# Performance work log

Measured on AMD Instinct MI355X. Metric: run time of the kernel, lower is better.

## Reference

```python
import jax, jax.numpy as jnp
import numpy as np

N, E, D, H = 50000, 800000, 128, 8
HD = D // H  # 16
HID = 512
EPS = 1e-5
SLOPE = 0.2  # DGL GATConv default negative_slope


def setup_inputs() -> dict:
    key = jax.random.key(0)
    ks = jax.random.split(key, 10)
    s = 0.1
    return {
        "x": jax.random.normal(ks[0], (N, D), jnp.float32),
        "src": jax.random.randint(ks[1], (E,), 0, N),
        "dst": jax.random.randint(ks[2], (E,), 0, N),
        "W": jax.random.normal(ks[3], (D, D), jnp.float32) * s,
        "attn_l": jax.random.normal(ks[4], (H, HD), jnp.float32) * s,
        "attn_r": jax.random.normal(ks[5], (H, HD), jnp.float32) * s,
        "bias_gat": jnp.zeros((D,), jnp.float32),
        "bn1_gamma": jnp.ones((D,), jnp.float32),
        "bn1_beta": jnp.zeros((D,), jnp.float32),
        "W1": jax.random.normal(ks[6], (D, HID), jnp.float32) * s,
        "b1": jnp.zeros((HID,), jnp.float32),
        "W2": jax.random.normal(ks[7], (HID, D), jnp.float32) * s,
        "b2": jnp.zeros((D,), jnp.float32),
        "bn2_gamma": jnp.ones((D,), jnp.float32),
        "bn2_beta": jnp.zeros((D,), jnp.float32),
    }


def _batchnorm(v, gamma, beta):
    # BatchNorm1d, training-mode forward (batch statistics, biased var)
    mu = v.mean(0)
    var = v.var(0)
    return (v - mu) * jax.lax.rsqrt(var + EPS) * gamma + beta


def reference(x, src, dst, W, attn_l, attn_r, bias_gat,
              bn1_gamma, bn1_beta, W1, b1, W2, b2, bn2_gamma, bn2_beta):
    n = x.shape[0]
    # GATConv: project + per-head attention logits
    feat = (x @ W).reshape(n, H, HD)                     # [N, H, hd]
    el = jnp.einsum('nhd,hd->nh', feat, attn_l)          # [N, H]
    er = jnp.einsum('nhd,hd->nh', feat, attn_r)          # [N, H]
    e = el[src] + er[dst]                                # [E, H]
    e = jnp.where(e > 0, e, SLOPE * e)                   # LeakyReLU
    # segment (edge) softmax over incoming edges of each dst node
    m = jax.ops.segment_max(e, dst, num_segments=n)      # [N, H]
    ee = jnp.exp(e - m[dst])
    denom = jax.ops.segment_sum(ee, dst, num_segments=n)
    alpha = ee / denom[dst]                              # [E, H]
    # weighted scatter-aggregate of source features
    msg = feat[src] * alpha[:, :, None]                  # [E, H, hd]
    agg = jax.ops.segment_sum(msg, dst, num_segments=n)  # [N, H, hd]
    h = agg.reshape(n, D) + bias_gat
    # BN -> Linear -> ReLU -> Linear -> BN
    h = _batchnorm(h, bn1_gamma, bn1_beta)
    h = jax.nn.relu(h @ W1 + b1) @ W2 + b2
    h = _batchnorm(h, bn2_gamma, bn2_beta)
    return h
```

## Files before the change

### kernel.cpp

```cpp
#include <hip/hip_runtime.h>
#include <math.h>

#define NHEAD 8
#define DD 128
#define HIDD 512
#define NB 768

typedef _Float16 half8 __attribute__((ext_vector_type(8)));
typedef _Float16 half4 __attribute__((ext_vector_type(4)));
typedef float floatx4 __attribute__((ext_vector_type(4)));

__device__ __forceinline__ int swz256(int row, int bytecol) {
  return row * 256 + (bytecol ^ ((row & 15) << 4));
}
__device__ __forceinline__ int swz512(int row, int bytecol) {
  return row * 512 + (bytecol ^ ((row & 15) << 4));
}

__global__ __launch_bounds__(256) void pack_kernel(
    const float* __restrict__ W, const float* __restrict__ W1,
    const float* __restrict__ W2, _Float16* __restrict__ WP,
    _Float16* __restrict__ W1TP, _Float16* __restrict__ W2P)
{
  int i = blockIdx.x * 256 + threadIdx.x;
  if (i < 4 * 128 * 4 * 8) {
    int ii = i & 7, l4 = (i >> 3) & 3, col = (i >> 5) & 127, kc = i >> 12;
    WP[i] = (_Float16)W[(kc * 32 + l4 * 8 + ii) * DD + col];
  }
  if (i < 65536) {
    int ii = i & 7, e = (i >> 3) & 63, tile = i >> 9;
    int l4 = e >> 4, l15 = e & 15, hb = tile >> 2, kc = tile & 3;
    W1TP[i] = (_Float16)W1[(size_t)(kc * 32 + l4 * 8 + ii) * HIDD + hb * 16 + l15];
  }
  if (i < 65536) {
    int ii = i & 7, e = (i >> 3) & 63, tile = i >> 9;
    int l4 = e >> 4, l15 = e & 15, c = tile >> 3, cb = tile & 7;
    int hidden = (ii < 4) ? (2 * c) * 16 + 4 * l4 + ii
                          : (2 * c + 1) * 16 + 4 * l4 + (ii - 4);
    W2P[i] = (_Float16)W2[(size_t)hidden * DD + cb * 16 + l15];
  }
}

__global__ __launch_bounds__(256) void feat_mfma_kernel(
    const float* __restrict__ x, const _Float16* __restrict__ WP,
    _Float16* __restrict__ feat16, int N, int T)
{
  __shared__ char xs[32 * 512];
  const int tid = threadIdx.x;
  const int wv = tid >> 6, lane = tid & 63;
  const int l15 = lane & 15, l4 = lane >> 4;
  const int row = tid >> 3, seg = tid & 7;

  int t = blockIdx.x;
  float4 pre[4];
  {
    const int n = t * 32 + row;
    const bool ok = (t < T) && (n < N);
    const float4* sp = (const float4*)(x + (size_t)n * DD + seg * 16);
    const float4 z = make_float4(0.f, 0.f, 0.f, 0.f);
    #pragma unroll
    for (int c = 0; c < 4; ++c) pre[c] = ok ? sp[c] : z;
  }

  for (; t < T; t += NB) {
    const int n0 = t * 32;
    #pragma unroll
    for (int c = 0; c < 4; ++c)
      *(float4*)(xs + swz512(row, seg * 64 + c * 16)) = pre[c];
    __syncthreads();

    floatx4 acc[2][2];
    #pragma unroll
    for (int mf = 0; mf < 2; ++mf) { acc[mf][0] = (floatx4)0.f; acc[mf][1] = (floatx4)0.f; }

    #pragma unroll
    for (int kc = 0; kc < 4; ++kc) {
      half8 b0 = *(const half8*)(WP + ((kc * 128 + wv * 32 + l15) * 4 + l4) * 8);
      half8 b1 = *(const half8*)(WP + ((kc * 128 + wv * 32 + 16 + l15) * 4 + l4) * 8);
      #pragma unroll
      for (int mf = 0; mf < 2; ++mf) {
        const int rr = mf * 16 + l15;
        float4 a0 = *(const float4*)(xs + swz512(rr, kc * 128 + l4 * 32));
        float4 a1 = *(const float4*)(xs + swz512(rr, kc * 128 + l4 * 32 + 16));
        half8 af;
        af[0] = (_Float16)a0.x; af[1] = (_Float16)a0.y; af[2] = (_Float16)a0.z; af[3] = (_Float16)a0.w;
        af[4] = (_Float16)a1.x; af[5] = (_Float16)a1.y; af[6] = (_Float16)a1.z; af[7] = (_Float16)a1.w;
        acc[mf][0] = __builtin_amdgcn_mfma_f32_16x16x32_f16(af, b0, acc[mf][0], 0, 0, 0);
        acc[mf][1] = __builtin_amdgcn_mfma_f32_16x16x32_f16(af, b1, acc[mf][1], 0, 0, 0);
      }
    }

    {
      const int tn = t + NB;
      const int n = tn * 32 + row;
      const bool ok = (tn < T) && (n < N);
      const float4* sp = (const float4*)(x + (size_t)n * DD + seg * 16);
      const float4 z = make_float4(0.f, 0.f, 0.f, 0.f);
      #pragma unroll
      for (int c = 0; c < 4; ++c) pre[c] = ok ? sp[c] : z;
    }

    #pragma unroll
    for (int mf = 0; mf < 2; ++mf) {
      #pragma unroll
      for (int r = 0; r < 4; ++r) {
        const int rown = n0 + mf * 16 + l4 * 4 + r;
        if (rown < N) {
          feat16[(size_t)rown * DD + wv * 32 + l15] = (_Float16)acc[mf][0][r];
          feat16[(size_t)rown * DD + wv * 32 + 16 + l15] = (_Float16)acc[mf][1][r];
        }
      }
    }
    __syncthreads();
  }
}

__global__ __launch_bounds__(256) void elr_kernel(
    const _Float16* __restrict__ feat16, const float* __restrict__ attn_l,
    const float* __restrict__ attn_r, float* __restrict__ el,
    float* __restrict__ er, int N)
{
  int gid = blockIdx.x * 256 + threadIdx.x;
  if (gid >= N * NHEAD) return;
  const int n = gid >> 3, h = gid & 7;
  const half8* fp = (const half8*)(feat16 + (size_t)n * DD + h * 16);
  half8 f0 = fp[0], f1 = fp[1];
  float sl = 0.f, sr = 0.f;
  #pragma unroll
  for (int d = 0; d < 8; ++d) {
    float v0 = (float)f0[d], v1 = (float)f1[d];
    sl = fmaf(v0, attn_l[h * 16 + d], sl);
    sl = fmaf(v1, attn_l[h * 16 + 8 + d], sl);
    sr = fmaf(v0, attn_r[h * 16 + d], sr);
    sr = fmaf(v1, attn_r[h * 16 + 8 + d], sr);
  }
  el[gid] = sl;
  er[gid] = sr;
}

__global__ __launch_bounds__(256) void count_kernel(const int* __restrict__ dst,
                                                    int* __restrict__ counts,
                                                    int* __restrict__ rank, int E)
{
  int e = blockIdx.x * 256 + threadIdx.x;
  if (e < E) rank[e] = atomicAdd(&counts[dst[e]], 1);
}

__global__ __launch_bounds__(256) void scan1_kernel(const int* __restrict__ counts,
                                                    int* __restrict__ offsets,
                                                    int* __restrict__ btot)
{
  __shared__ int wsum[4];
  const int lane = threadIdx.x & 63;
  const int wid = threadIdx.x >> 6;
  int4 c = *(const int4*)(counts + blockIdx.x * 1024 + threadIdx.x * 4);
  int q = c.x + c.y + c.z + c.w;
  int incl = q;
  #pragma unroll
  for (int d = 1; d < 64; d <<= 1) {
    int t = __shfl_up(incl, d, 64);
    if (lane >= d) incl += t;
  }
  if (lane == 63) wsum[wid] = incl;
  __syncthreads();
  int wprefix = 0;
  for (int w = 0; w < wid; ++w) wprefix += wsum[w];
  int excl = wprefix + incl - q;
  int4 o;
  o.x = excl; o.y = excl + c.x; o.z = o.y + c.y; o.w = o.z + c.z;
  *(int4*)(offsets + blockIdx.x * 1024 + threadIdx.x * 4) = o;
  if (threadIdx.x == 0) btot[blockIdx.x] = wsum[0] + wsum[1] + wsum[2] + wsum[3];
}

__global__ __launch_bounds__(64) void scan2_kernel(const int* __restrict__ btot,
                                                   int* __restrict__ bof, int nchunk)
{
  const int t = threadIdx.x;
  const int K = (nchunk + 63) >> 6;
  const int base = t * K;
  int s = 0;
  for (int i = 0; i < K; ++i) if (base + i < nchunk) s += btot[base + i];
  int incl = s;
  #pragma unroll
  for (int d = 1; d < 64; d <<= 1) {
    int tt = __shfl_up(incl, d, 64);
    if (t >= d) incl += tt;
  }
  int run = incl - s;
  for (int i = 0; i < K; ++i) if (base + i < nchunk) { bof[base + i] = run; run += btot[base + i]; }
}

__global__ __launch_bounds__(256) void fill_kernel(const int* __restrict__ src,
                                                   const int* __restrict__ dst,
                                                   const int* __restrict__ offsets,
                                                   const int* __restrict__ bof,
                                                   const int* __restrict__ rank,
                                                   int* __restrict__ srcl, int E)
{
  int e = blockIdx.x * 256 + threadIdx.x;
  if (e < E) {
    int d = dst[e];
    srcl[offsets[d] + bof[d >> 10] + rank[e]] = src[e];
  }
}

__global__ __launch_bounds__(256) void agg_kernel(
    const _Float16* __restrict__ feat16, const float* __restrict__ el,
    const float* __restrict__ er, const int* __restrict__ offsets,
    const int* __restrict__ bof, const int* __restrict__ srcl,
    const float* __restrict__ bias, float* __restrict__ hout, int N)
{
  int gid = blockIdx.x * 256 + threadIdx.x;
  if (gid >= N * 16) return;
  const int n = gid >> 4;
  const int sub = gid & 15;
  const int hh = sub >> 1;
  const int half = sub & 1;
  const int o0 = offsets[n] + bof[n >> 10];
  const int o1 = offsets[n + 1] + bof[(n + 1) >> 10];
  const int cnt = o1 - o0;
  const int mid = o0 + ((cnt + 1) >> 1);
  int j = half ? mid : o0;
  const int je = half ? o1 : mid;
  const float er_nh = er[n * NHEAD + hh];

  float s = 0.f;
  float a[16];
  #pragma unroll
  for (int d = 0; d < 16; ++d) a[d] = 0.f;

  for (; j + 1 < je; j += 2) {
    const int s0 = srcl[j], s1 = srcl[j + 1];
    float e0 = el[s0 * NHEAD + hh] + er_nh;
    float e1 = el[s1 * NHEAD + hh] + er_nh;
    const half8* f0p = (const half8*)(feat16 + (size_t)s0 * DD + hh * 16);
    const half8* f1p = (const half8*)(feat16 + (size_t)s1 * DD + hh * 16);
    e0 = e0 > 0.f ? e0 : 0.2f * e0;
    e1 = e1 > 0.f ? e1 : 0.2f * e1;
    const float pp0 = __expf(e0);
    const float pp1 = __expf(e1);
    half8 f00 = f0p[0], f01 = f0p[1];
    half8 f10 = f1p[0], f11 = f1p[1];
    s += pp0 + pp1;
    #pragma unroll
    for (int d = 0; d < 8; ++d) {
      a[d]     = fmaf(pp0, (float)f00[d], fmaf(pp1, (float)f10[d], a[d]));
      a[d + 8] = fmaf(pp0, (float)f01[d], fmaf(pp1, (float)f11[d], a[d + 8]));
    }
  }
  if (j < je) {
    const int s0 = srcl[j];
    float e0 = el[s0 * NHEAD + hh] + er_nh;
    e0 = e0 > 0.f ? e0 : 0.2f * e0;
    const float pp0 = __expf(e0);
    const half8* f0p = (const half8*)(feat16 + (size_t)s0 * DD + hh * 16);
    half8 f00 = f0p[0], f01 = f0p[1];
    s += pp0;
    #pragma unroll
    for (int d = 0; d < 8; ++d) {
      a[d]     = fmaf(pp0, (float)f00[d], a[d]);
      a[d + 8] = fmaf(pp0, (float)f01[d], a[d + 8]);
    }
  }

  s += __shfl_xor(s, 1, 64);
  #pragma unroll
  for (int d = 0; d < 16; ++d) a[d] += __shfl_xor(a[d], 1, 64);

  const float inv = (cnt > 0) ? 1.f / s : 0.f;
  const int cbase = hh * 16 + half * 8;
  float* op = hout + (size_t)n * DD + cbase;
  const float* bp = bias + cbase;
  const int abase = half * 8;
  float4 o0v, o1v;
  o0v.x = fmaf(a[abase + 0], inv, bp[0]);
  o0v.y = fmaf(a[abase + 1], inv, bp[1]);
  o0v.z = fmaf(a[abase + 2], inv, bp[2]);
  o0v.w = fmaf(a[abase + 3], inv, bp[3]);
  o1v.x = fmaf(a[abase + 4], inv, bp[4]);
  o1v.y = fmaf(a[abase + 5], inv, bp[5]);
  o1v.z = fmaf(a[abase + 6], inv, bp[6]);
  o1v.w = fmaf(a[abase + 7], inv, bp[7]);
  *(float4*)(op) = o0v;
  *(float4*)(op + 4) = o1v;
}

__global__ __launch_bounds__(256) void bnstats_kernel(
    const float* __restrict__ h, float* __restrict__ sums,
    float* __restrict__ sumsq, int N)
{
  __shared__ float rs[256], rss[256];
  const int c = threadIdx.x & 127;
  const int half = threadIdx.x >> 7;
  const int rowsPer = (N + gridDim.x - 1) / gridDim.x;
  const int r0 = blockIdx.x * rowsPer;
  const int r1 = min(N, r0 + rowsPer);
  float s = 0.f, ss = 0.f;
  for (int r = r0 + half; r < r1; r += 2) {
    float v = h[(size_t)r * DD + c];
    s += v; ss += v * v;
  }
  rs[threadIdx.x] = s; rss[threadIdx.x] = ss;
  __syncthreads();
  if (threadIdx.x < 128) {
    s = rs[threadIdx.x] + rs[threadIdx.x + 128];
    ss = rss[threadIdx.x] + rss[threadIdx.x + 128];
    atomicAdd(&sums[c], s);
    atomicAdd(&sumsq[c], ss);
  }
}

__global__ __launch_bounds__(128, 2) void mlp_mfma_kernel(
    const float* __restrict__ hbuf, const float* __restrict__ sum1,
    const float* __restrict__ ss1, const float* __restrict__ bn1_g,
    const float* __restrict__ bn1_b, const _Float16* __restrict__ W1TP,
    const _Float16* __restrict__ W2P, const float* __restrict__ b1,
    const float* __restrict__ b2, float* __restrict__ out, int N)
{
  __shared__ char myA[8192];
  __shared__ char xch[8192];
  const int tid = threadIdx.x;
  const int wv = tid >> 6;
  const int lane = tid & 63;
  const int l15 = lane & 15, l4 = lane >> 4;
  const int n0 = blockIdx.x * 32;
  if (n0 >= N) return;

  {
    const int c0 = (tid & 31) * 4;
    const int rq = tid >> 5;
    float sc[4], sh[4];
    #pragma unroll
    for (int jj = 0; jj < 4; ++jj) {
      float mean = sum1[c0 + jj] / (float)N;
      float var = ss1[c0 + jj] / (float)N - mean * mean;
      float s = bn1_g[c0 + jj] * rsqrtf(var + 1e-5f);
      sc[jj] = s; sh[jj] = bn1_b[c0 + jj] - mean * s;
    }
    #pragma unroll
    for (int it = 0; it < 8; ++it) {
      const int row = it * 4 + rq;
      const int n = n0 + row;
      float4 v = make_float4(0.f, 0.f, 0.f, 0.f);
      if (n < N) v = *(const float4*)(hbuf + (size_t)n * DD + c0);
      half4 hv;
      hv[0] = (_Float16)fmaf(v.x, sc[0], sh[0]);
      hv[1] = (_Float16)fmaf(v.y, sc[1], sh[1]);
      hv[2] = (_Float16)fmaf(v.z, sc[2], sh[2]);
      hv[3] = (_Float16)fmaf(v.w, sc[3], sh[3]);
      *(half4*)(myA + swz256(row, c0 * 2)) = hv;
    }
  }
  __syncthreads();

  half8 xf[2][4];
  #pragma unroll
  for (int nb = 0; nb < 2; ++nb)
    #pragma unroll
    for (int kc = 0; kc < 4; ++kc)
      xf[nb][kc] = *(const half8*)(myA + swz256(nb * 16 + l15, kc * 64 + l4 * 16));

  floatx4 acc2[2][8];
  #pragma unroll
  for (int nb = 0; nb < 2; ++nb)
    #pragma unroll
    for (int cb = 0; cb < 8; ++cb) acc2[nb][cb] = (floatx4)0.f;

  half8 a2s[8][2];
  #pragma unroll
  for (int c8 = 0; c8 < 8; ++c8) {
    const int c = wv * 8 + c8;
    floatx4 dA[2], dB[2];
    dA[0] = (floatx4)0.f; dA[1] = (floatx4)0.f;
    dB[0] = (floatx4)0.f; dB[1] = (floatx4)0.f;
    half8 wA[4], wB[4];
    #pragma unroll
    for (int kc = 0; kc < 4; ++kc) {
      wA[kc] = *(const half8*)(W1TP + (size_t)((2 * c) * 4 + kc) * 512 + (l4 * 16 + l15) * 8);
      wB[kc] = *(const half8*)(W1TP + (size_t)((2 * c + 1) * 4 + kc) * 512 + (l4 * 16 + l15) * 8);
    }
    __builtin_amdgcn_s_setprio(1);
    #pragma unroll
    for (int kc = 0; kc < 4; ++kc) {
      dA[0] = __builtin_amdgcn_mfma_f32_16x16x32_f16(wA[kc], xf[0][kc], dA[0], 0, 0, 0);
      dA[1] = __builtin_amdgcn_mfma_f32_16x16x32_f16(wA[kc], xf[1][kc], dA[1], 0, 0, 0);
      dB[0] = __builtin_amdgcn_mfma_f32_16x16x32_f16(wB[kc], xf[0][kc], dB[0], 0, 0, 0);
      dB[1] = __builtin_amdgcn_mfma_f32_16x16x32_f16(wB[kc], xf[1][kc], dB[1], 0, 0, 0);
    }
    __builtin_amdgcn_s_setprio(0);
    floatx4 bA = *(const floatx4*)&b1[(2 * c) * 16 + l4 * 4];
    floatx4 bB = *(const floatx4*)&b1[(2 * c + 1) * 16 + l4 * 4];
    #pragma unroll
    for (int nb = 0; nb < 2; ++nb) {
      #pragma unroll
      for (int r = 0; r < 4; ++r) {
        float vA = dA[nb][r] + bA[r];
        float vB = dB[nb][r] + bB[r];
        a2s[c8][nb][r]     = (_Float16)(vA > 0.f ? vA : 0.f);
        a2s[c8][nb][r + 4] = (_Float16)(vB > 0.f ? vB : 0.f);
      }
    }
  }
  #pragma unroll
  for (int c8 = 0; c8 < 8; ++c8) {
    const int c = wv * 8 + c8;
    half8 w2[8];
    #pragma unroll
    for (int cb = 0; cb < 8; ++cb)
      w2[cb] = *(const half8*)(W2P + (size_t)(c * 8 + cb) * 512 + (l4 * 16 + l15) * 8);
    __builtin_amdgcn_s_setprio(1);
    #pragma unroll
    for (int cb = 0; cb < 8; ++cb) {
      acc2[0][cb] = __builtin_amdgcn_mfma_f32_16x16x32_f16(a2s[c8][0], w2[cb], acc2[0][cb], 0, 0, 0);
      acc2[1][cb] = __builtin_amdgcn_mfma_f32_16x16x32_f16(a2s[c8][1], w2[cb], acc2[1][cb], 0, 0, 0);
    }
    __builtin_amdgcn_s_setprio(0);
  }

  if (wv == 1) {
    #pragma unroll
    for (int nb = 0; nb < 2; ++nb) {
      #pragma unroll
      for (int cb = 0; cb < 8; ++cb) {
        half4 hv;
        #pragma unroll
        for (int r = 0; r < 4; ++r) hv[r] = (_Float16)acc2[nb][cb][r];
        *(half4*)(xch + ((nb * 8 + cb) * 64 + lane) * 8) = hv;
      }
    }
  }
  __syncthreads();
  if (wv == 0) {
    float b2v[8];
    #pragma unroll
    for (int cb = 0; cb < 8; ++cb) b2v[cb] = b2[cb * 16 + l15];
    #pragma unroll
    for (int nb = 0; nb < 2; ++nb) {
      #pragma unroll
      for (int cb = 0; cb < 8; ++cb) {
        half4 hv = *(const half4*)(xch + ((nb * 8 + cb) * 64 + lane) * 8);
        #pragma unroll
        for (int r = 0; r < 4; ++r) acc2[nb][cb][r] += (float)hv[r];
      }
    }
    #pragma unroll
    for (int nb = 0; nb < 2; ++nb) {
      #pragma unroll
      for (int r = 0; r < 4; ++r) {
        const int rown = n0 + nb * 16 + l4 * 4 + r;
        if (rown < N) {
          #pragma unroll
          for (int cb = 0; cb < 8; ++cb)
            out[(size_t)rown * DD + cb * 16 + l15] = acc2[nb][cb][r] + b2v[cb];
        }
      }
    }
  }
}

__global__ __launch_bounds__(256) void applybn_kernel(
    float* __restrict__ out, const float* __restrict__ sum2,
    const float* __restrict__ ss2, const float* __restrict__ gamma,
    const float* __restrict__ beta, int N, int total4)
{
  __shared__ float sc[128], sh[128];
  if (threadIdx.x < 128) {
    int c = threadIdx.x;
    float mean = sum2[c] / (float)N;
    float var = ss2[c] / (float)N - mean * mean;
    float s = gamma[c] * rsqrtf(var + 1e-5f);
    sc[c] = s;
    sh[c] = beta[c] - mean * s;
  }
  __syncthreads();
  int i = blockIdx.x * 256 + threadIdx.x;
  const int stride = gridDim.x * 256;
  for (; i < total4; i += stride) {
    float4 v = ((float4*)out)[i];
    int c = (i & 31) * 4;
    float4 scv = *(const float4*)&sc[c];
    float4 shv = *(const float4*)&sh[c];
    v.x = fmaf(v.x, scv.x, shv.x); v.y = fmaf(v.y, scv.y, shv.y);
    v.z = fmaf(v.z, scv.z, shv.z); v.w = fmaf(v.w, scv.w, shv.w);
    ((float4*)out)[i] = v;
  }
}

extern "C" void kernel_launch(void* const* d_in, const int* in_sizes, int n_in,
                              void* d_out, int out_size, void* d_ws, size_t ws_size,
                              hipStream_t stream) {
  const float* x        = (const float*)d_in[0];
  const int*   src      = (const int*)d_in[1];
  const int*   dst      = (const int*)d_in[2];
  const float* W        = (const float*)d_in[3];
  const float* attn_l   = (const float*)d_in[4];
  const float* attn_r   = (const float*)d_in[5];
  const float* bias_gat = (const float*)d_in[6];
  const float* bn1_g    = (const float*)d_in[7];
  const float* bn1_b    = (const float*)d_in[8];
  const float* W1       = (const float*)d_in[9];
  const float* b1       = (const float*)d_in[10];
  const float* W2       = (const float*)d_in[11];
  const float* b2       = (const float*)d_in[12];
  const float* bn2_g    = (const float*)d_in[13];
  const float* bn2_b    = (const float*)d_in[14];
  float* out = (float*)d_out;

  const int N = in_sizes[0] / DD;
  const int E = in_sizes[1];
  const int NPAD = ((N + 1023) / 1024) * 1024;
  const int NCHUNK = NPAD / 1024;
  const int T = (N + 31) / 32;

  _Float16* feat16 = (_Float16*)d_ws;
  float* hbuf = (float*)(feat16 + (size_t)((N + 1) & ~1) * DD);
  float* el   = hbuf + (size_t)N * DD;
  float* er   = el + (size_t)N * NHEAD;
  int* counts = (int*)(er + (size_t)N * NHEAD);
  int* offsets = counts + NPAD;
  int* srcl   = offsets + NPAD;
  int* btot   = srcl + E;
  int* bof    = btot + 64;
  float* stats = (float*)(bof + 64);
  float* sum1 = stats, *ss1 = stats + 128;
  float* sum2 = stats + 256, *ss2 = stats + 384;
  _Float16* WP   = (_Float16*)(stats + 1024);
  _Float16* W1TP = WP + 4 * 128 * 32;
  _Float16* W2P  = W1TP + 65536;
  int* rank = (int*)hbuf;

  hipMemsetAsync(counts, 0, (size_t)NPAD * sizeof(int), stream);
  hipMemsetAsync(stats, 0, 512 * sizeof(float), stream);

  pack_kernel<<<256, 256, 0, stream>>>(W, W1, W2, WP, W1TP, W2P);
  feat_mfma_kernel<<<NB, 256, 0, stream>>>(x, WP, feat16, N, T);
  elr_kernel<<<(N * NHEAD + 255) / 256, 256, 0, stream>>>(feat16, attn_l, attn_r, el, er, N);
  count_kernel<<<(E + 255) / 256, 256, 0, stream>>>(dst, counts, rank, E);
  scan1_kernel<<<NCHUNK, 256, 0, stream>>>(counts, offsets, btot);
  scan2_kernel<<<1, 64, 0, stream>>>(btot, bof, NCHUNK);
  fill_kernel<<<(E + 255) / 256, 256, 0, stream>>>(src, dst, offsets, bof, rank, srcl, E);
  agg_kernel<<<(N * 16 + 255) / 256, 256, 0, stream>>>(feat16, el, er, offsets, bof,
                                                       srcl, bias_gat, hbuf, N);
  bnstats_kernel<<<256, 256, 0, stream>>>(hbuf, sum1, ss1, N);
  mlp_mfma_kernel<<<T, 128, 0, stream>>>(hbuf, sum1, ss1, bn1_g, bn1_b, W1TP, W2P,
                                         b1, b2, out, N);
  bnstats_kernel<<<256, 256, 0, stream>>>(out, sum2, ss2, N);
  applybn_kernel<<<2048, 256, 0, stream>>>(out, sum2, ss2, bn2_g, bn2_b, N, N * DD / 4);
}
```

Before: 230.1 us.

## Unroll GAT aggregation by four edges and split MLP hidden dim across four waves

The edge aggregation loop now handles four source edges per iteration instead of two, putting more independent gathers in flight per thread. The MLP kernel goes from two to four waves per block, each owning a quarter of the 512 hidden units. This halves per-wave MFMA and register work, and the three non-leader waves reduce their partial outputs through a larger shared-memory exchange buffer. The cost is three times the LDS for the exchange, a longer serial reduction in wave 0, and extra fp16 rounding of partials.

```diff
diff --git a/kernel.cpp b/kernel.cpp
--- a/kernel.cpp
+++ b/kernel.cpp
@@ -229,37 +229,46 @@
   #pragma unroll
   for (int d = 0; d < 16; ++d) a[d] = 0.f;
 
-  for (; j + 1 < je; j += 2) {
-    const int s0 = srcl[j], s1 = srcl[j + 1];
+  for (; j + 3 < je; j += 4) {
+    const int s0 = srcl[j], s1 = srcl[j + 1], s2 = srcl[j + 2], s3 = srcl[j + 3];
     float e0 = el[s0 * NHEAD + hh] + er_nh;
     float e1 = el[s1 * NHEAD + hh] + er_nh;
+    float e2 = el[s2 * NHEAD + hh] + er_nh;
+    float e3 = el[s3 * NHEAD + hh] + er_nh;
     const half8* f0p = (const half8*)(feat16 + (size_t)s0 * DD + hh * 16);
     const half8* f1p = (const half8*)(feat16 + (size_t)s1 * DD + hh * 16);
+    const half8* f2p = (const half8*)(feat16 + (size_t)s2 * DD + hh * 16);
+    const half8* f3p = (const half8*)(feat16 + (size_t)s3 * DD + hh * 16);
     e0 = e0 > 0.f ? e0 : 0.2f * e0;
     e1 = e1 > 0.f ? e1 : 0.2f * e1;
-    const float pp0 = __expf(e0);
-    const float pp1 = __expf(e1);
+    e2 = e2 > 0.f ? e2 : 0.2f * e2;
+    e3 = e3 > 0.f ? e3 : 0.2f * e3;
+    const float p0 = __expf(e0), p1 = __expf(e1), p2 = __expf(e2), p3 = __expf(e3);
     half8 f00 = f0p[0], f01 = f0p[1];
     half8 f10 = f1p[0], f11 = f1p[1];
-    s += pp0 + pp1;
+    half8 f20 = f2p[0], f21 = f2p[1];
+    half8 f30 = f3p[0], f31 = f3p[1];
+    s += (p0 + p1) + (p2 + p3);
     #pragma unroll
     for (int d = 0; d < 8; ++d) {
-      a[d]     = fmaf(pp0, (float)f00[d], fmaf(pp1, (float)f10[d], a[d]));
-      a[d + 8] = fmaf(pp0, (float)f01[d], fmaf(pp1, (float)f11[d], a[d + 8]));
-    }
-  }
-  if (j < je) {
+      float t0 = fmaf(p0, (float)f00[d], fmaf(p1, (float)f10[d], a[d]));
+      a[d] = fmaf(p2, (float)f20[d], fmaf(p3, (float)f30[d], t0));
+      float t1 = fmaf(p0, (float)f01[d], fmaf(p1, (float)f11[d], a[d + 8]));
+      a[d + 8] = fmaf(p2, (float)f21[d], fmaf(p3, (float)f31[d], t1));
+    }
+  }
+  for (; j < je; ++j) {
     const int s0 = srcl[j];
     float e0 = el[s0 * NHEAD + hh] + er_nh;
     e0 = e0 > 0.f ? e0 : 0.2f * e0;
-    const float pp0 = __expf(e0);
+    const float p0 = __expf(e0);
     const half8* f0p = (const half8*)(feat16 + (size_t)s0 * DD + hh * 16);
     half8 f00 = f0p[0], f01 = f0p[1];
-    s += pp0;
+    s += p0;
     #pragma unroll
     for (int d = 0; d < 8; ++d) {
-      a[d]     = fmaf(pp0, (float)f00[d], a[d]);
-      a[d + 8] = fmaf(pp0, (float)f01[d], a[d + 8]);
+      a[d]     = fmaf(p0, (float)f00[d], a[d]);
+      a[d + 8] = fmaf(p0, (float)f01[d], a[d + 8]);
     }
   }
 
@@ -310,7 +319,7 @@
   }
 }
 
-__global__ __launch_bounds__(128, 2) void mlp_mfma_kernel(
+__global__ __launch_bounds__(256, 2) void mlp_mfma_kernel(
     const float* __restrict__ hbuf, const float* __restrict__ sum1,
     const float* __restrict__ ss1, const float* __restrict__ bn1_g,
     const float* __restrict__ bn1_b, const _Float16* __restrict__ W1TP,
@@ -318,7 +327,7 @@
     const float* __restrict__ b2, float* __restrict__ out, int N)
 {
   __shared__ char myA[8192];
-  __shared__ char xch[8192];
+  __shared__ char xch[3 * 8192];
   const int tid = threadIdx.x;
   const int wv = tid >> 6;
   const int lane = tid & 63;
@@ -338,8 +347,8 @@
       sc[jj] = s; sh[jj] = bn1_b[c0 + jj] - mean * s;
     }
     #pragma unroll
-    for (int it = 0; it < 8; ++it) {
-      const int row = it * 4 + rq;
+    for (int it = 0; it < 4; ++it) {
+      const int row = it * 8 + rq;
       const int n = n0 + row;
       float4 v = make_float4(0.f, 0.f, 0.f, 0.f);
       if (n < N) v = *(const float4*)(hbuf + (size_t)n * DD + c0);
@@ -366,10 +375,10 @@
     #pragma unroll
     for (int cb = 0; cb < 8; ++cb) acc2[nb][cb] = (floatx4)0.f;
 
-  half8 a2s[8][2];
-  #pragma unroll
-  for (int c8 = 0; c8 < 8; ++c8) {
-    const int c = wv * 8 + c8;
+  half8 a2s[4][2];
+  #pragma unroll
+  for (int c8 = 0; c8 < 4; ++c8) {
+    const int c = wv * 4 + c8;
     floatx4 dA[2], dB[2];
     dA[0] = (floatx4)0.f; dA[1] = (floatx4)0.f;
     dB[0] = (floatx4)0.f; dB[1] = (floatx4)0.f;
@@ -402,8 +411,8 @@
     }
   }
   #pragma unroll
-  for (int c8 = 0; c8 < 8; ++c8) {
-    const int c = wv * 8 + c8;
+  for (int c8 = 0; c8 < 4; ++c8) {
+    const int c = wv * 4 + c8;
     half8 w2[8];
     #pragma unroll
     for (int cb = 0; cb < 8; ++cb)
@@ -417,7 +426,8 @@
     __builtin_amdgcn_s_setprio(0);
   }
 
-  if (wv == 1) {
+  if (wv != 0) {
+    char* myX = xch + (wv - 1) * 8192;
     #pragma unroll
     for (int nb = 0; nb < 2; ++nb) {
       #pragma unroll
@@ -425,7 +435,7 @@
         half4 hv;
         #pragma unroll
         for (int r = 0; r < 4; ++r) hv[r] = (_Float16)acc2[nb][cb][r];
-        *(half4*)(xch + ((nb * 8 + cb) * 64 + lane) * 8) = hv;
+        *(half4*)(myX + ((nb * 8 + cb) * 64 + lane) * 8) = hv;
       }
     }
   }
@@ -435,12 +445,15 @@
     #pragma unroll
     for (int cb = 0; cb < 8; ++cb) b2v[cb] = b2[cb * 16 + l15];
     #pragma unroll
-    for (int nb = 0; nb < 2; ++nb) {
-      #pragma unroll
-      for (int cb = 0; cb < 8; ++cb) {
-        half4 hv = *(const half4*)(xch + ((nb * 8 + cb) * 64 + lane) * 8);
+    for (int sw = 0; sw < 3; ++sw) {
+      #pragma unroll
+      for (int nb = 0; nb < 2; ++nb) {
         #pragma unroll
-        for (int r = 0; r < 4; ++r) acc2[nb][cb][r] += (float)hv[r];
+        for (int cb = 0; cb < 8; ++cb) {
+          half4 hv = *(const half4*)(xch + sw * 8192 + ((nb * 8 + cb) * 64 + lane) * 8);
+          #pragma unroll
+          for (int r = 0; r < 4; ++r) acc2[nb][cb][r] += (float)hv[r];
+        }
       }
     }
     #pragma unroll
@@ -542,7 +555,7 @@
   agg_kernel<<<(N * 16 + 255) / 256, 256, 0, stream>>>(feat16, el, er, offsets, bof,
                                                        srcl, bias_gat, hbuf, N);
   bnstats_kernel<<<256, 256, 0, stream>>>(hbuf, sum1, ss1, N);
-  mlp_mfma_kernel<<<T, 128, 0, stream>>>(hbuf, sum1, ss1, bn1_g, bn1_b, W1TP, W2P,
+  mlp_mfma_kernel<<<T, 256, 0, stream>>>(hbuf, sum1, ss1, bn1_g, bn1_b, W1TP, W2P,
                                          b1, b2, out, N);
   bnstats_kernel<<<256, 256, 0, stream>>>(out, sum2, ss2, N);
   applybn_kernel<<<2048, 256, 0, stream>>>(out, sum2, ss2, bn2_g, bn2_b, N, N * DD / 4);
```

Result: no change. 231.3 us (+0.5%).
